# Kernel optimization log

Measured on AMD Instinct MI355X. Metric: run time of the kernel, lower is better.

The kernel has to match this reference:

```python
import jax, jax.numpy as jnp
import numpy as np
import math

B, QL, HID = 4, 4, 4096          # batch, speculative q_len, hidden_size
NH, NKV, HD = 32, 8, 128         # attention heads, kv heads, head_dim
GROUPS = NH // NKV               # GQA repeat factor = 4
PRIOR = 4096                     # cached (prior) KV length
THETA = 1.0e6                    # Mixtral rope_theta


def setup_inputs() -> dict:
    key = jax.random.key(0)
    ks = jax.random.split(key, 7)
    hidden_states = jax.random.normal(ks[0], (B, QL, HID), jnp.float32)
    past_k = jax.random.normal(ks[1], (B, NKV, PRIOR, HD), jnp.float32)
    past_v = jax.random.normal(ks[2], (B, NKV, PRIOR, HD), jnp.float32)
    wq = jax.random.normal(ks[3], (HID, NH * HD), jnp.float32) * 0.02
    wk = jax.random.normal(ks[4], (HID, NKV * HD), jnp.float32) * 0.02
    wv = jax.random.normal(ks[5], (HID, NKV * HD), jnp.float32) * 0.02
    wo = jax.random.normal(ks[6], (NH * HD, HID), jnp.float32) * 0.02
    # prior mask: all cached positions visible
    attention_mask = jnp.ones((B, 1, QL, PRIOR), dtype=bool)
    # active mask: causal over the speculative window
    active_mask = jnp.broadcast_to(jnp.tril(jnp.ones((QL, QL), dtype=bool)), (B, 1, QL, QL))
    position_ids = jnp.broadcast_to(PRIOR + jnp.arange(QL, dtype=jnp.int64), (B, QL))
    return {"hidden_states": hidden_states, "past_k": past_k, "past_v": past_v,
            "wq": wq, "wk": wk, "wv": wv, "wo": wo,
            "attention_mask": attention_mask, "active_mask": active_mask,
            "position_ids": position_ids}


def _rotate_half(x):
    x1, x2 = jnp.split(x, 2, axis=-1)
    return jnp.concatenate([-x2, x1], axis=-1)


def _rope_cos_sin(position_ids):
    inv_freq = 1.0 / (THETA ** (jnp.arange(0, HD, 2, dtype=jnp.float32) / HD))  # [HD/2]
    freqs = position_ids.astype(jnp.float32)[..., None] * inv_freq              # [B,QL,HD/2]
    emb = jnp.concatenate([freqs, freqs], axis=-1)                              # [B,QL,HD]
    return jnp.cos(emb)[:, None], jnp.sin(emb)[:, None]                          # [B,1,QL,HD]


def reference(hidden_states, past_k, past_v, wq, wk, wv, wo,
              attention_mask, active_mask, position_ids):
    # fused QKV projection (no bias in Mixtral)
    q = (hidden_states @ wq).reshape(B, QL, NH, HD).transpose(0, 2, 1, 3)   # [B,NH,QL,HD]
    k = (hidden_states @ wk).reshape(B, QL, NKV, HD).transpose(0, 2, 1, 3)  # [B,NKV,QL,HD]
    v = (hidden_states @ wv).reshape(B, QL, NKV, HD).transpose(0, 2, 1, 3)
    # RoPE on Q and active K
    cos, sin = _rope_cos_sin(position_ids)
    q = q * cos + _rotate_half(q) * sin
    k = k * cos + _rotate_half(k) * sin
    # GQA repeat_kv
    k_prior = jnp.repeat(past_k, GROUPS, axis=1)  # [B,NH,PRIOR,HD]
    v_prior = jnp.repeat(past_v, GROUPS, axis=1)
    k_active = jnp.repeat(k, GROUPS, axis=1)      # [B,NH,QL,HD]
    v_active = jnp.repeat(v, GROUPS, axis=1)
    scale = 1.0 / math.sqrt(HD)
    neg = jnp.finfo(jnp.float32).min
    prior_scores = jnp.einsum('bhqd,bhkd->bhqk', q, k_prior) * scale
    prior_scores = jnp.where(attention_mask, prior_scores, neg)
    active_scores = jnp.einsum('bhqd,bhkd->bhqk', q, k_active) * scale
    active_scores = jnp.where(active_mask, active_scores, neg)   # is_speculation=True
    # decomposed softmax: shared max and shared divisor across prior/active
    max_score = jnp.maximum(prior_scores.max(-1, keepdims=True),
                            active_scores.max(-1, keepdims=True))
    prior_exp = jnp.exp(prior_scores - max_score)
    active_exp = jnp.exp(active_scores - max_score)
    divisor = prior_exp.sum(-1, keepdims=True) + active_exp.sum(-1, keepdims=True)
    attn = (jnp.einsum('bhqk,bhkd->bhqd', prior_exp / divisor, v_prior) +
            jnp.einsum('bhqk,bhkd->bhqd', active_exp / divisor, v_active))
    attn = attn.transpose(0, 2, 1, 3).reshape(B, QL, NH * HD)
    return attn @ wo
```

## Files before the change

### kernel.cpp

```cpp
#include <hip/hip_runtime.h>
#include <math.h>

#define NROWS 16
#define NCOLS 6144
#define HID   4096
#define NKV   8
#define HD    128
#define PRIOR 4096
#define NCH   32
#define CHUNK 128
#define SUB   64
#define KC1   128
#define NKC   32

__global__ __launch_bounds__(256)
void k_qkv_partial(const float* __restrict__ hid,
                   const float* __restrict__ wq,
                   const float* __restrict__ wk,
                   const float* __restrict__ wv,
                   float* __restrict__ part)
{
    const int t   = threadIdx.x;
    const int col = blockIdx.x * 256 + t;
    const int kc  = blockIdx.y;
    const int k0  = kc * KC1;
    __shared__ float sA[NROWS][KC1];
    for (int i = t; i < NROWS * KC1; i += 256) {
        const int r = i >> 7, kk = i & 127;
        sA[r][kk] = hid[(size_t)r * HID + k0 + kk];
    }
    const float* w; int wn, wcol;
    if (col < 4096)      { w = wq; wn = 4096; wcol = col; }
    else if (col < 5120) { w = wk; wn = 1024; wcol = col - 4096; }
    else                 { w = wv; wn = 1024; wcol = col - 5120; }
    const float* wp = w + wcol + (size_t)k0 * wn;
    __syncthreads();

    float acc[NROWS];
#pragma unroll
    for (int m = 0; m < NROWS; m++) acc[m] = 0.f;
#pragma unroll 2
    for (int kk = 0; kk < KC1; kk += 4) {
        const float w0 = wp[(size_t)(kk + 0) * wn];
        const float w1 = wp[(size_t)(kk + 1) * wn];
        const float w2 = wp[(size_t)(kk + 2) * wn];
        const float w3 = wp[(size_t)(kk + 3) * wn];
#pragma unroll
        for (int m = 0; m < NROWS; m++) {
            const float4 h4 = *(const float4*)(&sA[m][kk]);
            acc[m] = fmaf(h4.x, w0, fmaf(h4.y, w1, fmaf(h4.z, w2, fmaf(h4.w, w3, acc[m]))));
        }
    }
    float* po = part + (size_t)kc * (NROWS * NCOLS) + col;
#pragma unroll
    for (int m = 0; m < NROWS; m++) po[(size_t)m * NCOLS] = acc[m];
}

__global__ __launch_bounds__(256)
void k_reduce_rope(const float* __restrict__ part, float* __restrict__ qkv)
{
    const int tid = blockIdx.x * 256 + threadIdx.x;
    const double L64 = 0.21586735246819178;

    if (tid < 32768) {
        const int d = tid & 63, h = (tid >> 6) & 31, r = tid >> 11;
        const int c1 = h * HD + d;
        float s1 = 0.f, s2 = 0.f;
        for (int c = 0; c < NKC; c++) {
            const float* p = part + (size_t)c * (NROWS * NCOLS) + r * NCOLS + c1;
            s1 += p[0]; s2 += p[64];
        }
        const double ang = (double)(PRIOR + (r & 3)) * exp(-(double)d * L64);
        double sv, cv; sincos(ang, &sv, &cv);
        const float cf = (float)cv, sf = (float)sv, sc = 0.08838834764831845f;
        qkv[r * NCOLS + c1]      = (s1 * cf - s2 * sf) * sc;
        qkv[r * NCOLS + c1 + 64] = (s2 * cf + s1 * sf) * sc;
    } else if (tid < 40960) {
        const int idx = tid - 32768;
        const int d = idx & 63, kh = (idx >> 6) & 7, r = idx >> 9;
        const int c1 = 4096 + kh * HD + d;
        float s1 = 0.f, s2 = 0.f;
        for (int c = 0; c < NKC; c++) {
            const float* p = part + (size_t)c * (NROWS * NCOLS) + r * NCOLS + c1;
            s1 += p[0]; s2 += p[64];
        }
        const double ang = (double)(PRIOR + (r & 3)) * exp(-(double)d * L64);
        double sv, cv; sincos(ang, &sv, &cv);
        const float cf = (float)cv, sf = (float)sv;
        qkv[r * NCOLS + c1]      = s1 * cf - s2 * sf;
        qkv[r * NCOLS + c1 + 64] = s2 * cf + s1 * sf;
    } else {
        const int idx = tid - 40960;
        const int n = idx & 1023, r = idx >> 10;
        const int c1 = 5120 + n;
        float s = 0.f;
        for (int c = 0; c < NKC; c++)
            s += part[(size_t)c * (NROWS * NCOLS) + r * NCOLS + c1];
        qkv[r * NCOLS + c1] = s;
    }
}

__global__ __launch_bounds__(256, 4)
void k_attn_prior(const float* __restrict__ qkv,
                  const float* __restrict__ pk,
                  const float* __restrict__ pv,
                  float* __restrict__ part3)
{
    const int chunk = blockIdx.x, kvh = blockIdx.y, b = blockIdx.z;
    const int t = threadIdx.x;

    __shared__ float kT[SUB][132];
    __shared__ float pP[SUB][16];
    __shared__ float aS[16];

    const int key = t & 63;
    const int qg  = t >> 6;
    const int dpv = t & 127;
    const int rh  = t >> 7;

    const size_t kvoff = ((size_t)(b * NKV + kvh) * PRIOR + (size_t)chunk * CHUNK) * HD;
    const float* kbase = pk + kvoff;
    const float* vbase = pv + kvoff;

    const float* qr[4];
#pragma unroll
    for (int i = 0; i < 4; i++)
        qr[i] = qkv + (size_t)(b * 4 + i) * NCOLS + (kvh * 4 + qg) * HD;

    float m_r[4], l_r[4];
#pragma unroll
    for (int i = 0; i < 4; i++) { m_r[i] = -INFINITY; l_r[i] = 0.f; }
    float o[8] = {0.f,0.f,0.f,0.f,0.f,0.f,0.f,0.f};

    for (int st = 0; st < CHUNK / SUB; st++) {
#pragma unroll
        for (int p = 0; p < 8; p++) {
            const int i = p * 256 + t;
            const int kk = i >> 5, dl = (i & 31) * 4;
            const float4 k4 = *(const float4*)(kbase + (size_t)(st * SUB + kk) * HD + dl);
            *(float4*)(&kT[kk][dl]) = k4;
        }
        __syncthreads();
        float s0 = 0.f, s1 = 0.f, s2 = 0.f, s3 = 0.f;
#pragma unroll 2
        for (int d = 0; d < HD; d += 4) {
            const float4 k4 = *(const float4*)(&kT[key][d]);
            const float4 qa = *(const float4*)(qr[0] + d);
            const float4 qb = *(const float4*)(qr[1] + d);
            const float4 qc = *(const float4*)(qr[2] + d);
            const float4 qd = *(const float4*)(qr[3] + d);
            s0 = fmaf(qa.x,k4.x, fmaf(qa.y,k4.y, fmaf(qa.z,k4.z, fmaf(qa.w,k4.w, s0))));
            s1 = fmaf(qb.x,k4.x, fmaf(qb.y,k4.y, fmaf(qb.z,k4.z, fmaf(qb.w,k4.w, s1))));
            s2 = fmaf(qc.x,k4.x, fmaf(qc.y,k4.y, fmaf(qc.z,k4.z, fmaf(qc.w,k4.w, s2))));
            s3 = fmaf(qd.x,k4.x, fmaf(qd.y,k4.y, fmaf(qd.z,k4.z, fmaf(qd.w,k4.w, s3))));
        }
        float sv[4] = {s0, s1, s2, s3};
        float mx[4] = {s0, s1, s2, s3};
        for (int off = 32; off; off >>= 1) {
#pragma unroll
            for (int i = 0; i < 4; i++) mx[i] = fmaxf(mx[i], __shfl_xor(mx[i], off));
        }
        float pr[4], sm[4], al[4];
#pragma unroll
        for (int i = 0; i < 4; i++) {
            const float mn = fmaxf(m_r[i], mx[i]);
            pr[i] = __expf(sv[i] - mn);
            al[i] = __expf(m_r[i] - mn);
            m_r[i] = mn;
            sm[i] = pr[i];
        }
        *(float4*)(&pP[key][qg * 4]) = make_float4(pr[0], pr[1], pr[2], pr[3]);
        for (int off = 32; off; off >>= 1) {
#pragma unroll
            for (int i = 0; i < 4; i++) sm[i] += __shfl_xor(sm[i], off);
        }
#pragma unroll
        for (int i = 0; i < 4; i++) l_r[i] = l_r[i] * al[i] + sm[i];
        if (key == 0) {
#pragma unroll
            for (int i = 0; i < 4; i++) aS[qg * 4 + i] = al[i];
        }
        __syncthreads();
        float alv[8];
#pragma unroll
        for (int j = 0; j < 8; j++) alv[j] = aS[rh * 8 + j];
#pragma unroll
        for (int j = 0; j < 8; j++) o[j] *= alv[j];
        const float* vs = vbase + (size_t)st * SUB * HD + dpv;
#pragma unroll 8
        for (int k2 = 0; k2 < SUB; k2++) {
            const float v = vs[(size_t)k2 * HD];
            const float4 pa = *(const float4*)(&pP[k2][rh * 8]);
            const float4 pb = *(const float4*)(&pP[k2][rh * 8 + 4]);
            o[0] = fmaf(pa.x, v, o[0]); o[1] = fmaf(pa.y, v, o[1]);
            o[2] = fmaf(pa.z, v, o[2]); o[3] = fmaf(pa.w, v, o[3]);
            o[4] = fmaf(pb.x, v, o[4]); o[5] = fmaf(pb.y, v, o[5]);
            o[6] = fmaf(pb.z, v, o[6]); o[7] = fmaf(pb.w, v, o[7]);
        }
        __syncthreads();
    }
    float* pout = part3 + (size_t)((b * NKV + kvh) * NCH + chunk) * 2080;
    if (key == 0) {
#pragma unroll
        for (int i = 0; i < 4; i++) { pout[qg * 4 + i] = m_r[i]; pout[16 + qg * 4 + i] = l_r[i]; }
    }
#pragma unroll
    for (int j = 0; j < 8; j++)
        pout[32 + (rh * 8 + j) * HD + dpv] = o[j];
}

__global__ __launch_bounds__(256)
void k_combine(const float* __restrict__ qkv,
               const float* __restrict__ part3,
               float* __restrict__ attn)
{
    const int g = blockIdx.x & 3, kvh = (blockIdx.x >> 2) & 7, b = blockIdx.x >> 5;
    const int t = threadIdx.x;
    __shared__ float qL[4][128], kA[4][128], vA[4][128];
    __shared__ float mC[NCH][4], lC[NCH][4], fC[NCH][4];
    __shared__ float sAct[4][4], pA[4][4], invL[4];

    for (int i = t; i < 512; i += 256) {
        const int ql = i >> 7, d = i & 127;
        qL[ql][d] = qkv[(size_t)(b * 4 + ql) * NCOLS + (kvh * 4 + g) * HD + d];
        kA[ql][d] = qkv[(size_t)(b * 4 + ql) * NCOLS + 4096 + kvh * HD + d];
        vA[ql][d] = qkv[(size_t)(b * 4 + ql) * NCOLS + 5120 + kvh * HD + d];
    }
    const float* p3 = part3 + (size_t)(b * NKV + kvh) * NCH * 2080;
    for (int i = t; i < NCH * 4; i += 256) {
        const int c = i >> 2, lr = i & 3;
        mC[c][lr] = p3[c * 2080 + g * 4 + lr];
        lC[c][lr] = p3[c * 2080 + 16 + g * 4 + lr];
    }
    __syncthreads();
    if (t < 16) {
        const int lr = t >> 2, k = t & 3;
        float s = 0.f;
        for (int d = 0; d < HD; d++) s = fmaf(qL[lr][d], kA[k][d], s);
        sAct[lr][k] = s;
    }
    __syncthreads();
    if (t < 4) {
        const int lr = t;
        float M = -INFINITY;
        for (int c = 0; c < NCH; c++) M = fmaxf(M, mC[c][lr]);
        for (int k = 0; k <= lr; k++) M = fmaxf(M, sAct[lr][k]);
        float l = 0.f;
        for (int c = 0; c < NCH; c++) {
            const float f = __expf(mC[c][lr] - M);
            fC[c][lr] = f;
            l = fmaf(f, lC[c][lr], l);
        }
#pragma unroll
        for (int k = 0; k < 4; k++) {
            const float p = (k <= lr) ? __expf(sAct[lr][k] - M) : 0.f;
            pA[lr][k] = p; l += p;
        }
        invL[lr] = 1.f / l;
    }
    __syncthreads();

    const int d = t & 127, hr = t >> 7;
    const int lr0 = hr * 2, lr1 = hr * 2 + 1;
    float o0 = 0.f, o1 = 0.f;
    for (int c = 0; c < NCH; c++) {
        const float f0 = fC[c][lr0], f1 = fC[c][lr1];
        const float* pa = p3 + c * 2080 + 32 + (g * 4 + lr0) * HD + d;
        o0 = fmaf(f0, pa[0],  o0);
        o1 = fmaf(f1, pa[HD], o1);
    }
#pragma unroll
    for (int k = 0; k < 4; k++) {
        const float v = vA[k][d];
        o0 = fmaf(pA[lr0][k], v, o0);
        o1 = fmaf(pA[lr1][k], v, o1);
    }
    attn[(size_t)(b * 4 + lr0) * HID + (kvh * 4 + g) * HD + d] = o0 * invL[lr0];
    attn[(size_t)(b * 4 + lr1) * HID + (kvh * 4 + g) * HD + d] = o1 * invL[lr1];
}

__global__ __launch_bounds__(256)
void k_out_partial(const float* __restrict__ attn,
                   const float* __restrict__ wo,
                   float* __restrict__ part)
{
    const int t = threadIdx.x;
    const int col = blockIdx.x * 256 + t;
    const int kc = blockIdx.y;
    const int k0 = kc * KC1;
    __shared__ float sA[NROWS][KC1];
    for (int i = t; i < NROWS * KC1; i += 256) {
        const int r = i >> 7, kk = i & 127;
        sA[r][kk] = attn[(size_t)r * HID + k0 + kk];
    }
    const float* wp = wo + col + (size_t)k0 * HID;
    __syncthreads();

    float acc[NROWS];
#pragma unroll
    for (int m = 0; m < NROWS; m++) acc[m] = 0.f;
#pragma unroll 2
    for (int kk = 0; kk < KC1; kk += 4) {
        const float w0 = wp[(size_t)(kk + 0) * HID];
        const float w1 = wp[(size_t)(kk + 1) * HID];
        const float w2 = wp[(size_t)(kk + 2) * HID];
        const float w3 = wp[(size_t)(kk + 3) * HID];
#pragma unroll
        for (int m = 0; m < NROWS; m++) {
            const float4 h4 = *(const float4*)(&sA[m][kk]);
            acc[m] = fmaf(h4.x, w0, fmaf(h4.y, w1, fmaf(h4.z, w2, fmaf(h4.w, w3, acc[m]))));
        }
    }
    float* po = part + (size_t)kc * (NROWS * HID) + col;
#pragma unroll
    for (int m = 0; m < NROWS; m++) po[(size_t)m * HID] = acc[m];
}

__global__ __launch_bounds__(256)
void k_out_reduce(const float* __restrict__ part, float* __restrict__ out)
{
    const int tid = blockIdx.x * 256 + threadIdx.x;
    const float* p = part + (size_t)tid * 4;
    float4 s = make_float4(0.f, 0.f, 0.f, 0.f);
    for (int c = 0; c < NKC; c++) {
        const float4 a = *(const float4*)(p + (size_t)c * (NROWS * HID));
        s.x += a.x; s.y += a.y; s.z += a.z; s.w += a.w;
    }
    *(float4*)(out + (size_t)tid * 4) = s;
}

extern "C" void kernel_launch(void* const* d_in, const int* in_sizes, int n_in,
                              void* d_out, int out_size, void* d_ws, size_t ws_size,
                              hipStream_t stream)
{
    (void)in_sizes; (void)n_in; (void)out_size; (void)ws_size;
    const float* hid = (const float*)d_in[0];
    const float* pk  = (const float*)d_in[1];
    const float* pv  = (const float*)d_in[2];
    const float* wq  = (const float*)d_in[3];
    const float* wk  = (const float*)d_in[4];
    const float* wv  = (const float*)d_in[5];
    const float* wo  = (const float*)d_in[6];
    float* out = (float*)d_out;
    float* ws  = (float*)d_ws;

    float* P1   = ws;
    float* P3   = ws;
    float* P5   = ws;
    float* qkv  = ws + 3145728;
    float* attn = ws + 3244032;

    k_qkv_partial<<<dim3(24, NKC), 256, 0, stream>>>(hid, wq, wk, wv, P1);
    k_reduce_rope<<<224, 256, 0, stream>>>(P1, qkv);
    k_attn_prior<<<dim3(NCH, NKV, 4), 256, 0, stream>>>(qkv, pk, pv, P3);
    k_combine<<<128, 256, 0, stream>>>(qkv, P3, attn);
    k_out_partial<<<dim3(16, NKC), 256, 0, stream>>>(attn, wo, P5);
    k_out_reduce<<<64, 256, 0, stream>>>(P5, out);
}
```

Before: 368.0 us.

## Register-tile attention QK and PV, widen GEMV columns per thread

```diff
diff --git a/kernel.cpp b/kernel.cpp
--- a/kernel.cpp
+++ b/kernel.cpp
@@ -13,7 +13,7 @@
 #define KC1   128
 #define NKC   32
 
-__global__ __launch_bounds__(256)
+__global__ __launch_bounds__(128)
 void k_qkv_partial(const float* __restrict__ hid,
                    const float* __restrict__ wq,
                    const float* __restrict__ wk,
@@ -21,39 +21,35 @@
                    float* __restrict__ part)
 {
     const int t   = threadIdx.x;
-    const int col = blockIdx.x * 256 + t;
+    const int col = blockIdx.x * 256 + t * 2;
     const int kc  = blockIdx.y;
     const int k0  = kc * KC1;
-    __shared__ float sA[NROWS][KC1];
-    for (int i = t; i < NROWS * KC1; i += 256) {
-        const int r = i >> 7, kk = i & 127;
-        sA[r][kk] = hid[(size_t)r * HID + k0 + kk];
-    }
     const float* w; int wn, wcol;
     if (col < 4096)      { w = wq; wn = 4096; wcol = col; }
     else if (col < 5120) { w = wk; wn = 1024; wcol = col - 4096; }
     else                 { w = wv; wn = 1024; wcol = col - 5120; }
     const float* wp = w + wcol + (size_t)k0 * wn;
-    __syncthreads();
-
-    float acc[NROWS];
-#pragma unroll
-    for (int m = 0; m < NROWS; m++) acc[m] = 0.f;
+
+    float acc[NROWS][2];
+#pragma unroll
+    for (int m = 0; m < NROWS; m++) { acc[m][0] = 0.f; acc[m][1] = 0.f; }
 #pragma unroll 2
     for (int kk = 0; kk < KC1; kk += 4) {
-        const float w0 = wp[(size_t)(kk + 0) * wn];
-        const float w1 = wp[(size_t)(kk + 1) * wn];
-        const float w2 = wp[(size_t)(kk + 2) * wn];
-        const float w3 = wp[(size_t)(kk + 3) * wn];
+        const float2 w0 = *(const float2*)(wp + (size_t)(kk + 0) * wn);
+        const float2 w1 = *(const float2*)(wp + (size_t)(kk + 1) * wn);
+        const float2 w2 = *(const float2*)(wp + (size_t)(kk + 2) * wn);
+        const float2 w3 = *(const float2*)(wp + (size_t)(kk + 3) * wn);
 #pragma unroll
         for (int m = 0; m < NROWS; m++) {
-            const float4 h4 = *(const float4*)(&sA[m][kk]);
-            acc[m] = fmaf(h4.x, w0, fmaf(h4.y, w1, fmaf(h4.z, w2, fmaf(h4.w, w3, acc[m]))));
+            const float4 h4 = *(const float4*)(hid + (size_t)m * HID + k0 + kk);
+            acc[m][0] = fmaf(h4.x, w0.x, fmaf(h4.y, w1.x, fmaf(h4.z, w2.x, fmaf(h4.w, w3.x, acc[m][0]))));
+            acc[m][1] = fmaf(h4.x, w0.y, fmaf(h4.y, w1.y, fmaf(h4.z, w2.y, fmaf(h4.w, w3.y, acc[m][1]))));
         }
     }
     float* po = part + (size_t)kc * (NROWS * NCOLS) + col;
 #pragma unroll
-    for (int m = 0; m < NROWS; m++) po[(size_t)m * NCOLS] = acc[m];
+    for (int m = 0; m < NROWS; m++)
+        *(float2*)(po + (size_t)m * NCOLS) = make_float2(acc[m][0], acc[m][1]);
 }
 
 __global__ __launch_bounds__(256)
@@ -108,105 +104,176 @@
 {
     const int chunk = blockIdx.x, kvh = blockIdx.y, b = blockIdx.z;
     const int t = threadIdx.x;
-
-    __shared__ float kT[SUB][132];
-    __shared__ float pP[SUB][16];
-    __shared__ float aS[16];
-
-    const int key = t & 63;
-    const int qg  = t >> 6;
-    const int dpv = t & 127;
-    const int rh  = t >> 7;
+    const int lane = t & 63;
+
+    __shared__ float kT[128][64];
+    __shared__ float qT[128][16];
+    float* pP = &kT[88][0];
+    float* aS = &kT[108][0];
+
+    const int qt = t >> 6;
+    const int h  = (lane >> 4) & 3;
+    const int kt = lane & 15;
+
+    const int d4pv = t & 31;
+    const int kp   = (t >> 5) & 3;
+    const int rh   = t >> 7;
 
     const size_t kvoff = ((size_t)(b * NKV + kvh) * PRIOR + (size_t)chunk * CHUNK) * HD;
     const float* kbase = pk + kvoff;
     const float* vbase = pv + kvoff;
 
-    const float* qr[4];
-#pragma unroll
-    for (int i = 0; i < 4; i++)
-        qr[i] = qkv + (size_t)(b * 4 + i) * NCOLS + (kvh * 4 + qg) * HD;
+    for (int i = t; i < 2048; i += 256) {
+        const int r = i & 15, d = i >> 4;
+        const int ql = r & 3, g = r >> 2;
+        qT[d][r] = qkv[(size_t)(b * 4 + ql) * NCOLS + (kvh * 4 + g) * HD + d];
+    }
 
     float m_r[4], l_r[4];
 #pragma unroll
     for (int i = 0; i < 4; i++) { m_r[i] = -INFINITY; l_r[i] = 0.f; }
-    float o[8] = {0.f,0.f,0.f,0.f,0.f,0.f,0.f,0.f};
+    float o[8][4];
+#pragma unroll
+    for (int jr = 0; jr < 8; jr++)
+#pragma unroll
+        for (int jd = 0; jd < 4; jd++) o[jr][jd] = 0.f;
 
     for (int st = 0; st < CHUNK / SUB; st++) {
-#pragma unroll
-        for (int p = 0; p < 8; p++) {
-            const int i = p * 256 + t;
-            const int kk = i >> 5, dl = (i & 31) * 4;
-            const float4 k4 = *(const float4*)(kbase + (size_t)(st * SUB + kk) * HD + dl);
-            *(float4*)(&kT[kk][dl]) = k4;
+        {
+            const float* kr = kbase + (size_t)(st * SUB + lane) * HD + qt * 32;
+#pragma unroll
+            for (int i = 0; i < 8; i++) {
+                const float4 k4 = *(const float4*)(kr + i * 4);
+                const int d = qt * 32 + i * 4;
+                kT[d + 0][lane] = k4.x; kT[d + 1][lane] = k4.y;
+                kT[d + 2][lane] = k4.z; kT[d + 3][lane] = k4.w;
+            }
         }
         __syncthreads();
-        float s0 = 0.f, s1 = 0.f, s2 = 0.f, s3 = 0.f;
-#pragma unroll 2
-        for (int d = 0; d < HD; d += 4) {
-            const float4 k4 = *(const float4*)(&kT[key][d]);
-            const float4 qa = *(const float4*)(qr[0] + d);
-            const float4 qb = *(const float4*)(qr[1] + d);
-            const float4 qc = *(const float4*)(qr[2] + d);
-            const float4 qd = *(const float4*)(qr[3] + d);
-            s0 = fmaf(qa.x,k4.x, fmaf(qa.y,k4.y, fmaf(qa.z,k4.z, fmaf(qa.w,k4.w, s0))));
-            s1 = fmaf(qb.x,k4.x, fmaf(qb.y,k4.y, fmaf(qb.z,k4.z, fmaf(qb.w,k4.w, s1))));
-            s2 = fmaf(qc.x,k4.x, fmaf(qc.y,k4.y, fmaf(qc.z,k4.z, fmaf(qc.w,k4.w, s2))));
-            s3 = fmaf(qd.x,k4.x, fmaf(qd.y,k4.y, fmaf(qd.z,k4.z, fmaf(qd.w,k4.w, s3))));
-        }
-        float sv[4] = {s0, s1, s2, s3};
-        float mx[4] = {s0, s1, s2, s3};
-        for (int off = 32; off; off >>= 1) {
-#pragma unroll
-            for (int i = 0; i < 4; i++) mx[i] = fmaxf(mx[i], __shfl_xor(mx[i], off));
-        }
-        float pr[4], sm[4], al[4];
+
+        float a[4][4];
+#pragma unroll
+        for (int i = 0; i < 4; i++)
+#pragma unroll
+            for (int j = 0; j < 4; j++) a[i][j] = 0.f;
+#pragma unroll 4
+        for (int dd = 0; dd < 32; dd++) {
+            const int d = h * 32 + dd;
+            const float4 q4 = *(const float4*)(&qT[d][qt * 4]);
+            const float4 k4 = *(const float4*)(&kT[d][kt * 4]);
+            a[0][0]=fmaf(q4.x,k4.x,a[0][0]); a[0][1]=fmaf(q4.x,k4.y,a[0][1]); a[0][2]=fmaf(q4.x,k4.z,a[0][2]); a[0][3]=fmaf(q4.x,k4.w,a[0][3]);
+            a[1][0]=fmaf(q4.y,k4.x,a[1][0]); a[1][1]=fmaf(q4.y,k4.y,a[1][1]); a[1][2]=fmaf(q4.y,k4.z,a[1][2]); a[1][3]=fmaf(q4.y,k4.w,a[1][3]);
+            a[2][0]=fmaf(q4.z,k4.x,a[2][0]); a[2][1]=fmaf(q4.z,k4.y,a[2][1]); a[2][2]=fmaf(q4.z,k4.z,a[2][2]); a[2][3]=fmaf(q4.z,k4.w,a[2][3]);
+            a[3][0]=fmaf(q4.w,k4.x,a[3][0]); a[3][1]=fmaf(q4.w,k4.y,a[3][1]); a[3][2]=fmaf(q4.w,k4.z,a[3][2]); a[3][3]=fmaf(q4.w,k4.w,a[3][3]);
+        }
+        __syncthreads();
+
+#pragma unroll
+        for (int i = 0; i < 4; i++)
+#pragma unroll
+            for (int j = 0; j < 4; j++) {
+                float v = a[i][j];
+                v += __shfl_xor(v, 16);
+                v += __shfl_xor(v, 32);
+                a[i][j] = v;
+            }
+        float al[4], pr[4][4];
 #pragma unroll
         for (int i = 0; i < 4; i++) {
-            const float mn = fmaxf(m_r[i], mx[i]);
-            pr[i] = __expf(sv[i] - mn);
+            float mx = fmaxf(fmaxf(a[i][0], a[i][1]), fmaxf(a[i][2], a[i][3]));
+            mx = fmaxf(mx, __shfl_xor(mx, 1));
+            mx = fmaxf(mx, __shfl_xor(mx, 2));
+            mx = fmaxf(mx, __shfl_xor(mx, 4));
+            mx = fmaxf(mx, __shfl_xor(mx, 8));
+            const float mn = fmaxf(m_r[i], mx);
             al[i] = __expf(m_r[i] - mn);
             m_r[i] = mn;
-            sm[i] = pr[i];
-        }
-        *(float4*)(&pP[key][qg * 4]) = make_float4(pr[0], pr[1], pr[2], pr[3]);
-        for (int off = 32; off; off >>= 1) {
-#pragma unroll
-            for (int i = 0; i < 4; i++) sm[i] += __shfl_xor(sm[i], off);
-        }
-#pragma unroll
-        for (int i = 0; i < 4; i++) l_r[i] = l_r[i] * al[i] + sm[i];
-        if (key == 0) {
-#pragma unroll
-            for (int i = 0; i < 4; i++) aS[qg * 4 + i] = al[i];
+            float s = 0.f;
+#pragma unroll
+            for (int j = 0; j < 4; j++) { pr[i][j] = __expf(a[i][j] - mn); s += pr[i][j]; }
+            s += __shfl_xor(s, 1); s += __shfl_xor(s, 2);
+            s += __shfl_xor(s, 4); s += __shfl_xor(s, 8);
+            l_r[i] = l_r[i] * al[i] + s;
+        }
+        if (h == 0) {
+#pragma unroll
+            for (int j = 0; j < 4; j++)
+                *(float4*)(pP + (kt * 4 + j) * 20 + qt * 4) =
+                    make_float4(pr[0][j], pr[1][j], pr[2][j], pr[3][j]);
+        }
+        if (lane == 0) {
+#pragma unroll
+            for (int i = 0; i < 4; i++) aS[qt * 4 + i] = al[i];
         }
         __syncthreads();
-        float alv[8];
-#pragma unroll
-        for (int j = 0; j < 8; j++) alv[j] = aS[rh * 8 + j];
-#pragma unroll
-        for (int j = 0; j < 8; j++) o[j] *= alv[j];
-        const float* vs = vbase + (size_t)st * SUB * HD + dpv;
-#pragma unroll 8
-        for (int k2 = 0; k2 < SUB; k2++) {
-            const float v = vs[(size_t)k2 * HD];
-            const float4 pa = *(const float4*)(&pP[k2][rh * 8]);
-            const float4 pb = *(const float4*)(&pP[k2][rh * 8 + 4]);
-            o[0] = fmaf(pa.x, v, o[0]); o[1] = fmaf(pa.y, v, o[1]);
-            o[2] = fmaf(pa.z, v, o[2]); o[3] = fmaf(pa.w, v, o[3]);
-            o[4] = fmaf(pb.x, v, o[4]); o[5] = fmaf(pb.y, v, o[5]);
-            o[6] = fmaf(pb.z, v, o[6]); o[7] = fmaf(pb.w, v, o[7]);
+
+        {
+            float alv[8];
+#pragma unroll
+            for (int jr = 0; jr < 8; jr++) alv[jr] = aS[rh * 8 + jr];
+#pragma unroll
+            for (int jr = 0; jr < 8; jr++)
+#pragma unroll
+                for (int jd = 0; jd < 4; jd++) o[jr][jd] *= alv[jr];
+            const float* vs = vbase + (size_t)st * SUB * HD + d4pv * 4;
+#pragma unroll 4
+            for (int j = 0; j < 16; j++) {
+                const int key = kp * 16 + j;
+                const float4 v4 = *(const float4*)(vs + (size_t)key * HD);
+                const float4 pa = *(const float4*)(pP + key * 20 + rh * 8);
+                const float4 pb = *(const float4*)(pP + key * 20 + rh * 8 + 4);
+                const float pv8[8] = {pa.x, pa.y, pa.z, pa.w, pb.x, pb.y, pb.z, pb.w};
+                const float vv[4] = {v4.x, v4.y, v4.z, v4.w};
+#pragma unroll
+                for (int jr = 0; jr < 8; jr++)
+#pragma unroll
+                    for (int jd = 0; jd < 4; jd++)
+                        o[jr][jd] = fmaf(pv8[jr], vv[jd], o[jr][jd]);
+            }
         }
         __syncthreads();
     }
+
+    float* red = &kT[0][0];
+    const int rb = (rh * 32 + d4pv) * 36;
+    if (kp >= 2) {
+        float* wdst = red + (kp - 2) * 2304 + rb;
+#pragma unroll
+        for (int jr = 0; jr < 8; jr++)
+            *(float4*)(wdst + jr * 4) = make_float4(o[jr][0], o[jr][1], o[jr][2], o[jr][3]);
+    }
+    __syncthreads();
+    if (kp < 2) {
+        const float* rsrc = red + kp * 2304 + rb;
+#pragma unroll
+        for (int jr = 0; jr < 8; jr++) {
+            const float4 x = *(const float4*)(rsrc + jr * 4);
+            o[jr][0] += x.x; o[jr][1] += x.y; o[jr][2] += x.z; o[jr][3] += x.w;
+        }
+    }
+    __syncthreads();
+    if (kp == 1) {
+        float* wdst = red + rb;
+#pragma unroll
+        for (int jr = 0; jr < 8; jr++)
+            *(float4*)(wdst + jr * 4) = make_float4(o[jr][0], o[jr][1], o[jr][2], o[jr][3]);
+    }
+    __syncthreads();
+
     float* pout = part3 + (size_t)((b * NKV + kvh) * NCH + chunk) * 2080;
-    if (key == 0) {
-#pragma unroll
-        for (int i = 0; i < 4; i++) { pout[qg * 4 + i] = m_r[i]; pout[16 + qg * 4 + i] = l_r[i]; }
-    }
-#pragma unroll
-    for (int j = 0; j < 8; j++)
-        pout[32 + (rh * 8 + j) * HD + dpv] = o[j];
+    if (lane == 0) {
+#pragma unroll
+        for (int i = 0; i < 4; i++) { pout[qt * 4 + i] = m_r[i]; pout[16 + qt * 4 + i] = l_r[i]; }
+    }
+    if (kp == 0) {
+        const float* rsrc = red + rb;
+#pragma unroll
+        for (int jr = 0; jr < 8; jr++) {
+            const float4 x = *(const float4*)(rsrc + jr * 4);
+            *(float4*)(pout + 32 + (size_t)(rh * 8 + jr) * HD + d4pv * 4) =
+                make_float4(o[jr][0] + x.x, o[jr][1] + x.y, o[jr][2] + x.z, o[jr][3] + x.w);
+        }
+    }
 }
 
 __global__ __launch_bounds__(256)
@@ -279,41 +346,37 @@
     attn[(size_t)(b * 4 + lr1) * HID + (kvh * 4 + g) * HD + d] = o1 * invL[lr1];
 }
 
-__global__ __launch_bounds__(256)
+__global__ __launch_bounds__(128)
 void k_out_partial(const float* __restrict__ attn,
                    const float* __restrict__ wo,
                    float* __restrict__ part)
 {
     const int t = threadIdx.x;
-    const int col = blockIdx.x * 256 + t;
+    const int col = blockIdx.x * 256 + t * 2;
     const int kc = blockIdx.y;
     const int k0 = kc * KC1;
-    __shared__ float sA[NROWS][KC1];
-    for (int i = t; i < NROWS * KC1; i += 256) {
-        const int r = i >> 7, kk = i & 127;
-        sA[r][kk] = attn[(size_t)r * HID + k0 + kk];
-    }
     const float* wp = wo + col + (size_t)k0 * HID;
-    __syncthreads();
-
-    float acc[NROWS];
-#pragma unroll
-    for (int m = 0; m < NROWS; m++) acc[m] = 0.f;
+
+    float acc[NROWS][2];
+#pragma unroll
+    for (int m = 0; m < NROWS; m++) { acc[m][0] = 0.f; acc[m][1] = 0.f; }
 #pragma unroll 2
     for (int kk = 0; kk < KC1; kk += 4) {
-        const float w0 = wp[(size_t)(kk + 0) * HID];
-        const float w1 = wp[(size_t)(kk + 1) * HID];
-        const float w2 = wp[(size_t)(kk + 2) * HID];
-        const float w3 = wp[(size_t)(kk + 3) * HID];
+        const float2 w0 = *(const float2*)(wp + (size_t)(kk + 0) * HID);
+        const float2 w1 = *(const float2*)(wp + (size_t)(kk + 1) * HID);
+        const float2 w2 = *(const float2*)(wp + (size_t)(kk + 2) * HID);
+        const float2 w3 = *(const float2*)(wp + (size_t)(kk + 3) * HID);
 #pragma unroll
         for (int m = 0; m < NROWS; m++) {
-            const float4 h4 = *(const float4*)(&sA[m][kk]);
-            acc[m] = fmaf(h4.x, w0, fmaf(h4.y, w1, fmaf(h4.z, w2, fmaf(h4.w, w3, acc[m]))));
+            const float4 h4 = *(const float4*)(attn + (size_t)m * HID + k0 + kk);
+            acc[m][0] = fmaf(h4.x, w0.x, fmaf(h4.y, w1.x, fmaf(h4.z, w2.x, fmaf(h4.w, w3.x, acc[m][0]))));
+            acc[m][1] = fmaf(h4.x, w0.y, fmaf(h4.y, w1.y, fmaf(h4.z, w2.y, fmaf(h4.w, w3.y, acc[m][1]))));
         }
     }
     float* po = part + (size_t)kc * (NROWS * HID) + col;
 #pragma unroll
-    for (int m = 0; m < NROWS; m++) po[(size_t)m * HID] = acc[m];
+    for (int m = 0; m < NROWS; m++)
+        *(float2*)(po + (size_t)m * HID) = make_float2(acc[m][0], acc[m][1]);
 }
 
 __global__ __launch_bounds__(256)
@@ -350,10 +413,10 @@
     float* qkv  = ws + 3145728;
     float* attn = ws + 3244032;
 
-    k_qkv_partial<<<dim3(24, NKC), 256, 0, stream>>>(hid, wq, wk, wv, P1);
+    k_qkv_partial<<<dim3(24, NKC), 128, 0, stream>>>(hid, wq, wk, wv, P1);
     k_reduce_rope<<<224, 256, 0, stream>>>(P1, qkv);
     k_attn_prior<<<dim3(NCH, NKV, 4), 256, 0, stream>>>(qkv, pk, pv, P3);
     k_combine<<<128, 256, 0, stream>>>(qkv, P3, attn);
-    k_out_partial<<<dim3(16, NKC), 256, 0, stream>>>(attn, wo, P5);
+    k_out_partial<<<dim3(16, NKC), 128, 0, stream>>>(attn, wo, P5);
     k_out_reduce<<<64, 256, 0, stream>>>(P5, out);
 }
```

Result: faster. 321.5 us (-12.6%).

## Retile GEMV, attention, combine and reduce kernels with float4 register tiles

Applied to the files above, without the earlier changes.

```diff
diff --git a/kernel.cpp b/kernel.cpp
--- a/kernel.cpp
+++ b/kernel.cpp
@@ -13,47 +13,54 @@
 #define KC1   128
 #define NKC   32
 
-__global__ __launch_bounds__(256)
+__global__ __launch_bounds__(256, 4)
 void k_qkv_partial(const float* __restrict__ hid,
                    const float* __restrict__ wq,
                    const float* __restrict__ wk,
                    const float* __restrict__ wv,
                    float* __restrict__ part)
 {
-    const int t   = threadIdx.x;
-    const int col = blockIdx.x * 256 + t;
-    const int kc  = blockIdx.y;
-    const int k0  = kc * KC1;
+    const int t = threadIdx.x, lane = t & 63, w = t >> 6;
+    const int tile = blockIdx.x, kc = blockIdx.y, k0 = kc * KC1;
     __shared__ float sA[NROWS][KC1];
-    for (int i = t; i < NROWS * KC1; i += 256) {
-        const int r = i >> 7, kk = i & 127;
-        sA[r][kk] = hid[(size_t)r * HID + k0 + kk];
-    }
-    const float* w; int wn, wcol;
-    if (col < 4096)      { w = wq; wn = 4096; wcol = col; }
-    else if (col < 5120) { w = wk; wn = 1024; wcol = col - 4096; }
-    else                 { w = wv; wn = 1024; wcol = col - 5120; }
-    const float* wp = w + wcol + (size_t)k0 * wn;
-    __syncthreads();
-
-    float acc[NROWS];
-#pragma unroll
-    for (int m = 0; m < NROWS; m++) acc[m] = 0.f;
-#pragma unroll 2
+    for (int i = t; i < 512; i += 256) {
+        const int r = i >> 5, kk = (i & 31) * 4;
+        *(float4*)(&sA[r][kk]) = *(const float4*)(hid + (size_t)r * HID + k0 + kk);
+    }
+    const int col = tile * 256 + lane * 4;
+    const float* wsel; int wn, wcol;
+    if (tile < 16)      { wsel = wq; wn = 4096; wcol = col; }
+    else if (tile < 20) { wsel = wk; wn = 1024; wcol = col - 4096; }
+    else                { wsel = wv; wn = 1024; wcol = col - 5120; }
+    const float* wp = wsel + (size_t)k0 * wn + wcol;
+    __syncthreads();
+
+    float acc[4][4];
+#pragma unroll
+    for (int i = 0; i < 4; i++)
+#pragma unroll
+        for (int j = 0; j < 4; j++) acc[i][j] = 0.f;
+
+#pragma unroll 4
     for (int kk = 0; kk < KC1; kk += 4) {
-        const float w0 = wp[(size_t)(kk + 0) * wn];
-        const float w1 = wp[(size_t)(kk + 1) * wn];
-        const float w2 = wp[(size_t)(kk + 2) * wn];
-        const float w3 = wp[(size_t)(kk + 3) * wn];
-#pragma unroll
-        for (int m = 0; m < NROWS; m++) {
-            const float4 h4 = *(const float4*)(&sA[m][kk]);
-            acc[m] = fmaf(h4.x, w0, fmaf(h4.y, w1, fmaf(h4.z, w2, fmaf(h4.w, w3, acc[m]))));
+        const float4 w0 = *(const float4*)(wp + (size_t)(kk + 0) * wn);
+        const float4 w1 = *(const float4*)(wp + (size_t)(kk + 1) * wn);
+        const float4 w2 = *(const float4*)(wp + (size_t)(kk + 2) * wn);
+        const float4 w3 = *(const float4*)(wp + (size_t)(kk + 3) * wn);
+#pragma unroll
+        for (int i = 0; i < 4; i++) {
+            const float4 a = *(const float4*)(&sA[w * 4 + i][kk]);
+            acc[i][0] = fmaf(a.x, w0.x, fmaf(a.y, w1.x, fmaf(a.z, w2.x, fmaf(a.w, w3.x, acc[i][0]))));
+            acc[i][1] = fmaf(a.x, w0.y, fmaf(a.y, w1.y, fmaf(a.z, w2.y, fmaf(a.w, w3.y, acc[i][1]))));
+            acc[i][2] = fmaf(a.x, w0.z, fmaf(a.y, w1.z, fmaf(a.z, w2.z, fmaf(a.w, w3.z, acc[i][2]))));
+            acc[i][3] = fmaf(a.x, w0.w, fmaf(a.y, w1.w, fmaf(a.z, w2.w, fmaf(a.w, w3.w, acc[i][3]))));
         }
     }
     float* po = part + (size_t)kc * (NROWS * NCOLS) + col;
 #pragma unroll
-    for (int m = 0; m < NROWS; m++) po[(size_t)m * NCOLS] = acc[m];
+    for (int i = 0; i < 4; i++)
+        *(float4*)(po + (size_t)(w * 4 + i) * NCOLS) =
+            make_float4(acc[i][0], acc[i][1], acc[i][2], acc[i][3]);
 }
 
 __global__ __launch_bounds__(256)
@@ -107,48 +114,46 @@
                   float* __restrict__ part3)
 {
     const int chunk = blockIdx.x, kvh = blockIdx.y, b = blockIdx.z;
-    const int t = threadIdx.x;
-
-    __shared__ float kT[SUB][132];
-    __shared__ float pP[SUB][16];
-    __shared__ float aS[16];
-
-    const int key = t & 63;
-    const int qg  = t >> 6;
-    const int dpv = t & 127;
-    const int rh  = t >> 7;
+    const int t = threadIdx.x, lane = t & 63;
+
+    __shared__ float qR[NROWS][132];
+    __shared__ float pP[SUB][20];
+    __shared__ float aS[NROWS];
+
+    const int qt = t >> 6;
+    const int d4 = t & 31;
+    const int rp = t >> 5;
 
     const size_t kvoff = ((size_t)(b * NKV + kvh) * PRIOR + (size_t)chunk * CHUNK) * HD;
     const float* kbase = pk + kvoff;
     const float* vbase = pv + kvoff;
 
-    const float* qr[4];
-#pragma unroll
-    for (int i = 0; i < 4; i++)
-        qr[i] = qkv + (size_t)(b * 4 + i) * NCOLS + (kvh * 4 + qg) * HD;
+    for (int i = t; i < 2048; i += 256) {
+        const int d = i & 127, r = i >> 4 >> 3;
+        const int ql = r & 3, g = r >> 2;
+        qR[r][d] = qkv[(size_t)(b * 4 + ql) * NCOLS + (kvh * 4 + g) * HD + d];
+    }
 
     float m_r[4], l_r[4];
 #pragma unroll
     for (int i = 0; i < 4; i++) { m_r[i] = -INFINITY; l_r[i] = 0.f; }
-    float o[8] = {0.f,0.f,0.f,0.f,0.f,0.f,0.f,0.f};
+    float o[2][4] = {{0.f,0.f,0.f,0.f},{0.f,0.f,0.f,0.f}};
+    __syncthreads();
 
     for (int st = 0; st < CHUNK / SUB; st++) {
-#pragma unroll
-        for (int p = 0; p < 8; p++) {
-            const int i = p * 256 + t;
-            const int kk = i >> 5, dl = (i & 31) * 4;
-            const float4 k4 = *(const float4*)(kbase + (size_t)(st * SUB + kk) * HD + dl);
-            *(float4*)(&kT[kk][dl]) = k4;
-        }
-        __syncthreads();
+        const float* kr = kbase + (size_t)(st * SUB + lane) * HD;
+        const float* q0 = &qR[qt * 4 + 0][0];
+        const float* q1 = &qR[qt * 4 + 1][0];
+        const float* q2 = &qR[qt * 4 + 2][0];
+        const float* q3 = &qR[qt * 4 + 3][0];
         float s0 = 0.f, s1 = 0.f, s2 = 0.f, s3 = 0.f;
-#pragma unroll 2
+#pragma unroll 8
         for (int d = 0; d < HD; d += 4) {
-            const float4 k4 = *(const float4*)(&kT[key][d]);
-            const float4 qa = *(const float4*)(qr[0] + d);
-            const float4 qb = *(const float4*)(qr[1] + d);
-            const float4 qc = *(const float4*)(qr[2] + d);
-            const float4 qd = *(const float4*)(qr[3] + d);
+            const float4 k4 = *(const float4*)(kr + d);
+            const float4 qa = *(const float4*)(q0 + d);
+            const float4 qb = *(const float4*)(q1 + d);
+            const float4 qc = *(const float4*)(q2 + d);
+            const float4 qd = *(const float4*)(q3 + d);
             s0 = fmaf(qa.x,k4.x, fmaf(qa.y,k4.y, fmaf(qa.z,k4.z, fmaf(qa.w,k4.w, s0))));
             s1 = fmaf(qb.x,k4.x, fmaf(qb.y,k4.y, fmaf(qb.z,k4.z, fmaf(qb.w,k4.w, s1))));
             s2 = fmaf(qc.x,k4.x, fmaf(qc.y,k4.y, fmaf(qc.z,k4.z, fmaf(qc.w,k4.w, s2))));
@@ -169,44 +174,47 @@
             m_r[i] = mn;
             sm[i] = pr[i];
         }
-        *(float4*)(&pP[key][qg * 4]) = make_float4(pr[0], pr[1], pr[2], pr[3]);
+        *(float4*)(&pP[lane][qt * 4]) = make_float4(pr[0], pr[1], pr[2], pr[3]);
         for (int off = 32; off; off >>= 1) {
 #pragma unroll
             for (int i = 0; i < 4; i++) sm[i] += __shfl_xor(sm[i], off);
         }
 #pragma unroll
         for (int i = 0; i < 4; i++) l_r[i] = l_r[i] * al[i] + sm[i];
-        if (key == 0) {
-#pragma unroll
-            for (int i = 0; i < 4; i++) aS[qg * 4 + i] = al[i];
+        if (lane == 0) {
+#pragma unroll
+            for (int i = 0; i < 4; i++) aS[qt * 4 + i] = al[i];
         }
         __syncthreads();
-        float alv[8];
-#pragma unroll
-        for (int j = 0; j < 8; j++) alv[j] = aS[rh * 8 + j];
-#pragma unroll
-        for (int j = 0; j < 8; j++) o[j] *= alv[j];
-        const float* vs = vbase + (size_t)st * SUB * HD + dpv;
+
+        {
+            const float a0 = aS[rp * 2], a1 = aS[rp * 2 + 1];
+#pragma unroll
+            for (int j = 0; j < 4; j++) { o[0][j] *= a0; o[1][j] *= a1; }
+            const float* vs = vbase + (size_t)st * SUB * HD + d4 * 4;
 #pragma unroll 8
-        for (int k2 = 0; k2 < SUB; k2++) {
-            const float v = vs[(size_t)k2 * HD];
-            const float4 pa = *(const float4*)(&pP[k2][rh * 8]);
-            const float4 pb = *(const float4*)(&pP[k2][rh * 8 + 4]);
-            o[0] = fmaf(pa.x, v, o[0]); o[1] = fmaf(pa.y, v, o[1]);
-            o[2] = fmaf(pa.z, v, o[2]); o[3] = fmaf(pa.w, v, o[3]);
-            o[4] = fmaf(pb.x, v, o[4]); o[5] = fmaf(pb.y, v, o[5]);
-            o[6] = fmaf(pb.z, v, o[6]); o[7] = fmaf(pb.w, v, o[7]);
+            for (int key = 0; key < SUB; key++) {
+                const float4 v4 = *(const float4*)(vs + (size_t)key * HD);
+                const float p0 = pP[key][rp * 2];
+                const float p1 = pP[key][rp * 2 + 1];
+                o[0][0]=fmaf(p0,v4.x,o[0][0]); o[0][1]=fmaf(p0,v4.y,o[0][1]);
+                o[0][2]=fmaf(p0,v4.z,o[0][2]); o[0][3]=fmaf(p0,v4.w,o[0][3]);
+                o[1][0]=fmaf(p1,v4.x,o[1][0]); o[1][1]=fmaf(p1,v4.y,o[1][1]);
+                o[1][2]=fmaf(p1,v4.z,o[1][2]); o[1][3]=fmaf(p1,v4.w,o[1][3]);
+            }
         }
         __syncthreads();
     }
+
     float* pout = part3 + (size_t)((b * NKV + kvh) * NCH + chunk) * 2080;
-    if (key == 0) {
-#pragma unroll
-        for (int i = 0; i < 4; i++) { pout[qg * 4 + i] = m_r[i]; pout[16 + qg * 4 + i] = l_r[i]; }
-    }
-#pragma unroll
-    for (int j = 0; j < 8; j++)
-        pout[32 + (rh * 8 + j) * HD + dpv] = o[j];
+    if (lane == 0) {
+#pragma unroll
+        for (int i = 0; i < 4; i++) { pout[qt * 4 + i] = m_r[i]; pout[16 + qt * 4 + i] = l_r[i]; }
+    }
+#pragma unroll
+    for (int j = 0; j < 2; j++)
+        *(float4*)(pout + 32 + (size_t)(rp * 2 + j) * HD + d4 * 4) =
+            make_float4(o[j][0], o[j][1], o[j][2], o[j][3]);
 }
 
 __global__ __launch_bounds__(256)
@@ -214,9 +222,10 @@
                const float* __restrict__ part3,
                float* __restrict__ attn)
 {
-    const int g = blockIdx.x & 3, kvh = (blockIdx.x >> 2) & 7, b = blockIdx.x >> 5;
+    const int g = blockIdx.x & 3, dh = blockIdx.x >> 2;
+    const int kvh = blockIdx.y, b = blockIdx.z;
     const int t = threadIdx.x;
-    __shared__ float qL[4][128], kA[4][128], vA[4][128];
+    __shared__ float qL[4][128], kA[4][128], vA[4][64];
     __shared__ float mC[NCH][4], lC[NCH][4], fC[NCH][4];
     __shared__ float sAct[4][4], pA[4][4], invL[4];
 
@@ -224,7 +233,10 @@
         const int ql = i >> 7, d = i & 127;
         qL[ql][d] = qkv[(size_t)(b * 4 + ql) * NCOLS + (kvh * 4 + g) * HD + d];
         kA[ql][d] = qkv[(size_t)(b * 4 + ql) * NCOLS + 4096 + kvh * HD + d];
-        vA[ql][d] = qkv[(size_t)(b * 4 + ql) * NCOLS + 5120 + kvh * HD + d];
+    }
+    {
+        const int ql = t >> 6, d = t & 63;
+        vA[ql][d] = qkv[(size_t)(b * 4 + ql) * NCOLS + 5120 + kvh * HD + dh * 64 + d];
     }
     const float* p3 = part3 + (size_t)(b * NKV + kvh) * NCH * 2080;
     for (int i = t; i < NCH * 4; i += 256) {
@@ -260,73 +272,68 @@
     }
     __syncthreads();
 
-    const int d = t & 127, hr = t >> 7;
-    const int lr0 = hr * 2, lr1 = hr * 2 + 1;
-    float o0 = 0.f, o1 = 0.f;
-    for (int c = 0; c < NCH; c++) {
-        const float f0 = fC[c][lr0], f1 = fC[c][lr1];
-        const float* pa = p3 + c * 2080 + 32 + (g * 4 + lr0) * HD + d;
-        o0 = fmaf(f0, pa[0],  o0);
-        o1 = fmaf(f1, pa[HD], o1);
-    }
-#pragma unroll
-    for (int k = 0; k < 4; k++) {
-        const float v = vA[k][d];
-        o0 = fmaf(pA[lr0][k], v, o0);
-        o1 = fmaf(pA[lr1][k], v, o1);
-    }
-    attn[(size_t)(b * 4 + lr0) * HID + (kvh * 4 + g) * HD + d] = o0 * invL[lr0];
-    attn[(size_t)(b * 4 + lr1) * HID + (kvh * 4 + g) * HD + d] = o1 * invL[lr1];
-}
-
-__global__ __launch_bounds__(256)
+    const int d2 = t & 63, lr = t >> 6;
+    const float* pb = p3 + 32 + (size_t)(g * 4 + lr) * HD + dh * 64 + d2;
+    float o = 0.f;
+    for (int c = 0; c < NCH; c++)
+        o = fmaf(fC[c][lr], pb[(size_t)c * 2080], o);
+#pragma unroll
+    for (int k = 0; k < 4; k++)
+        o = fmaf(pA[lr][k], vA[k][d2], o);
+    attn[(size_t)(b * 4 + lr) * HID + (kvh * 4 + g) * HD + dh * 64 + d2] = o * invL[lr];
+}
+
+__global__ __launch_bounds__(256, 4)
 void k_out_partial(const float* __restrict__ attn,
                    const float* __restrict__ wo,
                    float* __restrict__ part)
 {
-    const int t = threadIdx.x;
-    const int col = blockIdx.x * 256 + t;
-    const int kc = blockIdx.y;
-    const int k0 = kc * KC1;
+    const int t = threadIdx.x, lane = t & 63, w = t >> 6;
+    const int tile = blockIdx.x, kc = blockIdx.y, k0 = kc * KC1;
     __shared__ float sA[NROWS][KC1];
-    for (int i = t; i < NROWS * KC1; i += 256) {
-        const int r = i >> 7, kk = i & 127;
-        sA[r][kk] = attn[(size_t)r * HID + k0 + kk];
-    }
-    const float* wp = wo + col + (size_t)k0 * HID;
-    __syncthreads();
-
-    float acc[NROWS];
-#pragma unroll
-    for (int m = 0; m < NROWS; m++) acc[m] = 0.f;
-#pragma unroll 2
+    for (int i = t; i < 512; i += 256) {
+        const int r = i >> 5, kk = (i & 31) * 4;
+        *(float4*)(&sA[r][kk]) = *(const float4*)(attn + (size_t)r * HID + k0 + kk);
+    }
+    const int col = tile * 256 + lane * 4;
+    const float* wp = wo + (size_t)k0 * HID + col;
+    __syncthreads();
+
+    float acc[4][4];
+#pragma unroll
+    for (int i = 0; i < 4; i++)
+#pragma unroll
+        for (int j = 0; j < 4; j++) acc[i][j] = 0.f;
+
+#pragma unroll 4
     for (int kk = 0; kk < KC1; kk += 4) {
-        const float w0 = wp[(size_t)(kk + 0) * HID];
-        const float w1 = wp[(size_t)(kk + 1) * HID];
-        const float w2 = wp[(size_t)(kk + 2) * HID];
-        const float w3 = wp[(size_t)(kk + 3) * HID];
-#pragma unroll
-        for (int m = 0; m < NROWS; m++) {
-            const float4 h4 = *(const float4*)(&sA[m][kk]);
-            acc[m] = fmaf(h4.x, w0, fmaf(h4.y, w1, fmaf(h4.z, w2, fmaf(h4.w, w3, acc[m]))));
+        const float4 w0 = *(const float4*)(wp + (size_t)(kk + 0) * HID);
+        const float4 w1 = *(const float4*)(wp + (size_t)(kk + 1) * HID);
+        const float4 w2 = *(const float4*)(wp + (size_t)(kk + 2) * HID);
+        const float4 w3 = *(const float4*)(wp + (size_t)(kk + 3) * HID);
+#pragma unroll
+        for (int i = 0; i < 4; i++) {
+            const float4 a = *(const float4*)(&sA[w * 4 + i][kk]);
+            acc[i][0] = fmaf(a.x, w0.x, fmaf(a.y, w1.x, fmaf(a.z, w2.x, fmaf(a.w, w3.x, acc[i][0]))));
+            acc[i][1] = fmaf(a.x, w0.y, fmaf(a.y, w1.y, fmaf(a.z, w2.y, fmaf(a.w, w3.y, acc[i][1]))));
+            acc[i][2] = fmaf(a.x, w0.z, fmaf(a.y, w1.z, fmaf(a.z, w2.z, fmaf(a.w, w3.z, acc[i][2]))));
+            acc[i][3] = fmaf(a.x, w0.w, fmaf(a.y, w1.w, fmaf(a.z, w2.w, fmaf(a.w, w3.w, acc[i][3]))));
         }
     }
     float* po = part + (size_t)kc * (NROWS * HID) + col;
 #pragma unroll
-    for (int m = 0; m < NROWS; m++) po[(size_t)m * HID] = acc[m];
+    for (int i = 0; i < 4; i++)
+        *(float4*)(po + (size_t)(w * 4 + i) * HID) =
+            make_float4(acc[i][0], acc[i][1], acc[i][2], acc[i][3]);
 }
 
 __global__ __launch_bounds__(256)
 void k_out_reduce(const float* __restrict__ part, float* __restrict__ out)
 {
     const int tid = blockIdx.x * 256 + threadIdx.x;
-    const float* p = part + (size_t)tid * 4;
-    float4 s = make_float4(0.f, 0.f, 0.f, 0.f);
-    for (int c = 0; c < NKC; c++) {
-        const float4 a = *(const float4*)(p + (size_t)c * (NROWS * HID));
-        s.x += a.x; s.y += a.y; s.z += a.z; s.w += a.w;
-    }
-    *(float4*)(out + (size_t)tid * 4) = s;
+    float s = 0.f;
+    for (int c = 0; c < NKC; c++) s += part[(size_t)c * (NROWS * HID) + tid];
+    out[tid] = s;
 }
 
 extern "C" void kernel_launch(void* const* d_in, const int* in_sizes, int n_in,
@@ -353,7 +360,7 @@
     k_qkv_partial<<<dim3(24, NKC), 256, 0, stream>>>(hid, wq, wk, wv, P1);
     k_reduce_rope<<<224, 256, 0, stream>>>(P1, qkv);
     k_attn_prior<<<dim3(NCH, NKV, 4), 256, 0, stream>>>(qkv, pk, pv, P3);
-    k_combine<<<128, 256, 0, stream>>>(qkv, P3, attn);
+    k_combine<<<dim3(8, 8, 4), 256, 0, stream>>>(qkv, P3, attn);
     k_out_partial<<<dim3(16, NKC), 256, 0, stream>>>(attn, wo, P5);
-    k_out_reduce<<<64, 256, 0, stream>>>(P5, out);
-}
+    k_out_reduce<<<256, 256, 0, stream>>>(P5, out);
+}
```

New measurement: 400.9 us. 1.09x slower.
